# Kernel optimization log

Hardware: AMD Instinct MI355X
Metric: run time of the kernel (lower is better)

## Reference

```python
import jax, jax.numpy as jnp
import numpy as np


def setup_inputs() -> dict:
    key = jax.random.key(0)
    k1, k2 = jax.random.split(key)
    x = jax.random.normal(k1, (16, 64, 224, 224), dtype=jnp.float32)
    # conv weight [out=1, in=2, kh=7, kw=7]; init roughly mimics small-normal init
    conv_w = jax.random.normal(k2, (1, 2, 7, 7), dtype=jnp.float32) * 0.01
    conv_b = jnp.zeros((1,), dtype=jnp.float32)
    return {"x": x, "conv_w": conv_w, "conv_b": conv_b}


def reference(x, conv_w, conv_b):
    # channel-wise mean and max -> [B, 2, H, W]
    avg_out = jnp.mean(x, axis=1, keepdims=True)
    max_out = jnp.max(x, axis=1, keepdims=True)
    feat = jnp.concatenate([avg_out, max_out], axis=1)
    # 2->1 channel 7x7 conv, padding 3 (same)
    y = jax.lax.conv_general_dilated(
        feat, conv_w,
        window_strides=(1, 1),
        padding=((3, 3), (3, 3)),
        dimension_numbers=("NCHW", "OIHW", "NCHW"),
    ) + conv_b[None, :, None, None]
    # sigmoid gate broadcast-multiplied back onto x
    return jax.nn.sigmoid(y) * x
```

## Files before the change

### kernel.cpp

```cpp
#include <hip/hip_runtime.h>
#include <math.h>

#define BB 16
#define CC 64
#define HH 224
#define WW 224
#define HWSZ (HH * WW)
#define HW4 (HWSZ / 4)
#define W4 (WW / 4)

typedef float f32x4 __attribute__((ext_vector_type(4)));

#define TA 256
#define NPIX (BB * HW4)
#define NBLKA (NPIX / TA)

__global__ __launch_bounds__(TA) void reduce_kernel(const float* __restrict__ x,
                                                    float* __restrict__ feat) {
    const int idx = blockIdx.x * TA + threadIdx.x;
    const int b   = idx / HW4;
    const int p   = idx - b * HW4;
    const f32x4* xp = reinterpret_cast<const f32x4*>(x) + (size_t)b * (CC * HW4) + p;

    f32x4 s = {0.f, 0.f, 0.f, 0.f};
    f32x4 m = {-INFINITY, -INFINITY, -INFINITY, -INFINITY};
#pragma unroll 16
    for (int c = 0; c < CC; ++c) {
        f32x4 u = xp[(size_t)c * HW4];
        s += u;
        m[0] = fmaxf(m[0], u[0]); m[1] = fmaxf(m[1], u[1]);
        m[2] = fmaxf(m[2], u[2]); m[3] = fmaxf(m[3], u[3]);
    }
    f32x4* fav = reinterpret_cast<f32x4*>(feat);
    f32x4* fmx = fav + NPIX;
    fav[idx] = s * (1.0f / 64.0f);
    fmx[idx] = m;
}

#define R 7
#define TILES (HH / R)
#define FR (R + 6)
#define FW 240
#define TC 256
#define NBLKC (BB * TILES)

__global__ __launch_bounds__(TC) void conv_kernel(const float* __restrict__ feat,
                                                  const float* __restrict__ cw,
                                                  const float* __restrict__ cb,
                                                  float* __restrict__ gate) {
    __shared__ float fa[FR * FW];
    __shared__ float fm[FR * FW];
    __shared__ float wt[98];

    const int blk = blockIdx.x;
    const int b   = blk >> 5;
    const int tb  = blk & 31;
    const int h0  = tb * R;
    const int t   = threadIdx.x;

    for (int i = t; i < FR * FW; i += TC) { fa[i] = 0.f; fm[i] = 0.f; }
    if (t < 98) wt[t] = cw[t];
    __syncthreads();

    const f32x4* fav = reinterpret_cast<const f32x4*>(feat) + (size_t)b * HW4;
    const f32x4* fmx = fav + NPIX;
    for (int q = t; q < 2 * FR * W4; q += TC) {
        int plane = (q >= FR * W4);
        int p  = plane ? q - FR * W4 : q;
        int pr = p / W4;
        int pc = p - pr * W4;
        int gh = h0 - 3 + pr;
        if ((unsigned)gh >= (unsigned)HH) continue;
        f32x4 u = (plane ? fmx : fav)[gh * W4 + pc];
        float* dst = (plane ? fm : fa) + pr * FW + 3 + pc * 4;
        dst[0] = u[0]; dst[1] = u[1]; dst[2] = u[2]; dst[3] = u[3];
    }
    __syncthreads();

    const float bias = cb[0];
    float* gb = gate + (size_t)b * HWSZ + (size_t)h0 * WW;
    for (int p = t; p < R * WW; p += TC) {
        int r = p / WW;
        int w = p - r * WW;
        float acc = bias;
#pragma unroll
        for (int kh = 0; kh < 7; ++kh) {
            int ro = (r + kh) * FW + w;
#pragma unroll
            for (int kw = 0; kw < 7; ++kw) {
                acc = fmaf(fa[ro + kw], wt[kh * 7 + kw], acc);
                acc = fmaf(fm[ro + kw], wt[49 + kh * 7 + kw], acc);
            }
        }
        gb[p] = 1.0f / (1.0f + expf(-acc));
    }
}

#define TM 256
#define CSPL 4
#define CPG (CC / CSPL)
#define CHUNKS (HW4 / TM)
#define NBLKM (BB * CSPL * CHUNKS)

__global__ __launch_bounds__(TM) void mul_kernel(const float* __restrict__ x,
                                                 const float* __restrict__ gate,
                                                 float* __restrict__ out) {
    const int blk   = blockIdx.x;
    const int chunk = blk % CHUNKS;
    const int cg    = (blk / CHUNKS) % CSPL;
    const int b     = blk / (CHUNKS * CSPL);
    const int p     = chunk * TM + threadIdx.x;

    const f32x4 g = reinterpret_cast<const f32x4*>(gate)[(size_t)b * HW4 + p];

    const size_t base = ((size_t)b * CC + cg * CPG) * HW4 + p;
    const f32x4* xp = reinterpret_cast<const f32x4*>(x) + base;
    f32x4*       op = reinterpret_cast<f32x4*>(out) + base;
#pragma unroll
    for (int c = 0; c < CPG; ++c) {
        f32x4 v = xp[(size_t)c * HW4];
        v *= g;
        __builtin_nontemporal_store(v, op + (size_t)c * HW4);
    }
}

extern "C" void kernel_launch(void* const* d_in, const int* in_sizes, int n_in,
                              void* d_out, int out_size, void* d_ws, size_t ws_size,
                              hipStream_t stream) {
    const float* x  = (const float*)d_in[0];
    const float* cw = (const float*)d_in[1];
    const float* cb = (const float*)d_in[2];
    float* out  = (float*)d_out;
    float* feat = (float*)d_ws;
    float* gate = feat + (size_t)2 * BB * HWSZ;

    reduce_kernel<<<NBLKA, TA, 0, stream>>>(x, feat);
    conv_kernel<<<NBLKC, TC, 0, stream>>>(feat, cw, cb, gate);
    mul_kernel<<<NBLKM, TM, 0, stream>>>(x, gate, out);
}
```

Measured before the change: 388.3 us.

## Pad feature planes in reduce and compute conv directly from global with register tiling

Result: no change. 392.4 us (+1.1%).

```diff
diff --git a/kernel.cpp b/kernel.cpp
--- a/kernel.cpp
+++ b/kernel.cpp
@@ -8,6 +8,12 @@
 #define HWSZ (HH * WW)
 #define HW4 (HWSZ / 4)
 #define W4 (WW / 4)
+
+#define PROWS (HH + 6)
+#define PW4 60
+#define PPLANE (PROWS * PW4)
+#define NPADC 1256
+#define NPADT (BB * NPADC)
 
 typedef float f32x4 __attribute__((ext_vector_type(4)));
 
@@ -31,69 +37,98 @@
         m[0] = fmaxf(m[0], u[0]); m[1] = fmaxf(m[1], u[1]);
         m[2] = fmaxf(m[2], u[2]); m[3] = fmaxf(m[3], u[3]);
     }
-    f32x4* fav = reinterpret_cast<f32x4*>(feat);
-    f32x4* fmx = fav + NPIX;
-    fav[idx] = s * (1.0f / 64.0f);
-    fmx[idx] = m;
+
+    f32x4* fa4 = reinterpret_cast<f32x4*>(feat);
+    f32x4* fm4 = fa4 + (size_t)BB * PPLANE;
+
+    const int h  = p / W4;
+    const int w4 = p - h * W4;
+    const size_t o = (size_t)(b * PROWS + (h + 3)) * PW4 + (w4 + 2);
+    fa4[o] = s * (1.0f / 64.0f);
+    fm4[o] = m;
+
+    if (idx < NPADT) {
+        const int pb = idx / NPADC;
+        int r = idx - pb * NPADC;
+        int prow, c4;
+        if (r < 360) {
+            int rr = r / 60;
+            c4 = r - rr * 60;
+            prow = (rr < 3) ? rr : 224 + rr;
+        } else {
+            int r2 = r - 360;
+            int rw = r2 >> 2;
+            int k  = r2 & 3;
+            prow = rw + 3;
+            c4 = (k < 2) ? k : 56 + k;
+        }
+        const size_t oz = (size_t)(pb * PROWS + prow) * PW4 + c4;
+        f32x4 z = {0.f, 0.f, 0.f, 0.f};
+        fa4[oz] = z;
+        fm4[oz] = z;
+    }
 }
 
-#define R 7
-#define TILES (HH / R)
-#define FR (R + 6)
-#define FW 240
-#define TC 256
-#define NBLKC (BB * TILES)
+#define TCN 256
+#define SEGS (WW / 8)
+#define NTHC (BB * HH * SEGS)
+#define NBLKC (NTHC / TCN)
 
-__global__ __launch_bounds__(TC) void conv_kernel(const float* __restrict__ feat,
-                                                  const float* __restrict__ cw,
-                                                  const float* __restrict__ cb,
-                                                  float* __restrict__ gate) {
-    __shared__ float fa[FR * FW];
-    __shared__ float fm[FR * FW];
-    __shared__ float wt[98];
+__global__ __launch_bounds__(TCN) void conv_kernel(const float* __restrict__ feat,
+                                                   const float* __restrict__ cw,
+                                                   const float* __restrict__ cb,
+                                                   float* __restrict__ gate) {
+    const int tid = blockIdx.x * TCN + threadIdx.x;
+    const int b   = tid / (HH * SEGS);
+    const int r   = tid - b * (HH * SEGS);
+    const int row = r / SEGS;
+    const int seg = r - row * SEGS;
+    const int w0  = seg * 8;
 
-    const int blk = blockIdx.x;
-    const int b   = blk >> 5;
-    const int tb  = blk & 31;
-    const int h0  = tb * R;
-    const int t   = threadIdx.x;
+    float wa[49], wb[49];
+#pragma unroll
+    for (int i = 0; i < 49; ++i) { wa[i] = cw[i]; wb[i] = cw[49 + i]; }
+    const float bias = cb[0];
 
-    for (int i = t; i < FR * FW; i += TC) { fa[i] = 0.f; fm[i] = 0.f; }
-    if (t < 98) wt[t] = cw[t];
-    __syncthreads();
+    const f32x4* fab = reinterpret_cast<const f32x4*>(feat) + (size_t)b * PPLANE;
+    const f32x4* fmb = fab + (size_t)BB * PPLANE;
 
-    const f32x4* fav = reinterpret_cast<const f32x4*>(feat) + (size_t)b * HW4;
-    const f32x4* fmx = fav + NPIX;
-    for (int q = t; q < 2 * FR * W4; q += TC) {
-        int plane = (q >= FR * W4);
-        int p  = plane ? q - FR * W4 : q;
-        int pr = p / W4;
-        int pc = p - pr * W4;
-        int gh = h0 - 3 + pr;
-        if ((unsigned)gh >= (unsigned)HH) continue;
-        f32x4 u = (plane ? fmx : fav)[gh * W4 + pc];
-        float* dst = (plane ? fm : fa) + pr * FW + 3 + pc * 4;
-        dst[0] = u[0]; dst[1] = u[1]; dst[2] = u[2]; dst[3] = u[3];
-    }
-    __syncthreads();
+    float acc[8];
+#pragma unroll
+    for (int j = 0; j < 8; ++j) acc[j] = bias;
 
-    const float bias = cb[0];
-    float* gb = gate + (size_t)b * HWSZ + (size_t)h0 * WW;
-    for (int p = t; p < R * WW; p += TC) {
-        int r = p / WW;
-        int w = p - r * WW;
-        float acc = bias;
 #pragma unroll
-        for (int kh = 0; kh < 7; ++kh) {
-            int ro = (r + kh) * FW + w;
+    for (int kh = 0; kh < 7; ++kh) {
+        const int bi = (row + kh) * PW4 + seg * 2 + 1;
+        float fA[16], fM[16];
 #pragma unroll
-            for (int kw = 0; kw < 7; ++kw) {
-                acc = fmaf(fa[ro + kw], wt[kh * 7 + kw], acc);
-                acc = fmaf(fm[ro + kw], wt[49 + kh * 7 + kw], acc);
+        for (int q = 0; q < 4; ++q) {
+            f32x4 a = fab[bi + q];
+            f32x4 mm = fmb[bi + q];
+#pragma unroll
+            for (int e = 0; e < 4; ++e) { fA[q * 4 + e] = a[e]; fM[q * 4 + e] = mm[e]; }
+        }
+#pragma unroll
+        for (int kw = 0; kw < 7; ++kw) {
+            const float w1 = wa[kh * 7 + kw];
+            const float w2 = wb[kh * 7 + kw];
+#pragma unroll
+            for (int j = 0; j < 8; ++j) {
+                acc[j] = fmaf(fA[1 + kw + j], w1, acc[j]);
+                acc[j] = fmaf(fM[1 + kw + j], w2, acc[j]);
             }
         }
-        gb[p] = 1.0f / (1.0f + expf(-acc));
     }
+
+    f32x4 g0, g1;
+#pragma unroll
+    for (int j = 0; j < 4; ++j) g0[j] = 1.0f / (1.0f + expf(-acc[j]));
+#pragma unroll
+    for (int j = 0; j < 4; ++j) g1[j] = 1.0f / (1.0f + expf(-acc[4 + j]));
+
+    f32x4* gb = reinterpret_cast<f32x4*>(gate) + ((size_t)b * HWSZ + (size_t)row * WW + w0) / 4;
+    gb[0] = g0;
+    gb[1] = g1;
 }
 
 #define TM 256
@@ -120,7 +155,7 @@
     for (int c = 0; c < CPG; ++c) {
         f32x4 v = xp[(size_t)c * HW4];
         v *= g;
-        __builtin_nontemporal_store(v, op + (size_t)c * HW4);
+        op[(size_t)c * HW4] = v;
     }
 }
 
@@ -132,9 +167,9 @@
     const float* cb = (const float*)d_in[2];
     float* out  = (float*)d_out;
     float* feat = (float*)d_ws;
-    float* gate = feat + (size_t)2 * BB * HWSZ;
+    float* gate = feat + (size_t)2 * BB * PPLANE * 4;
 
     reduce_kernel<<<NBLKA, TA, 0, stream>>>(x, feat);
-    conv_kernel<<<NBLKC, TC, 0, stream>>>(feat, cw, cb, gate);
+    conv_kernel<<<NBLKC, TCN, 0, stream>>>(feat, cw, cb, gate);
     mul_kernel<<<NBLKM, TM, 0, stream>>>(x, gate, out);
 }
```
